# Performance work log

Hardware: AMD Instinct MI355X
Metric: run time of the kernel (lower is better)

Reference implementation:

```python
import jax, jax.numpy as jnp
import numpy as np

BN_EPS = 1e-5

@jax.custom_vjp
def bsign(x):
    # forward: sign(x) (torch semantics: sign(0)=0, matched by jnp.sign)
    return jnp.sign(x)

def _bsign_fwd(x):
    return jnp.sign(x), x

def _bsign_bwd(x, g):
    # straight-through estimator: pass grad where |x| <= 1, zero elsewhere
    return (g * (jnp.abs(x) <= 1.0).astype(g.dtype),)

bsign.defvjp(_bsign_fwd, _bsign_bwd)


def setup_inputs() -> dict:
    key = jax.random.key(0)
    k1, k2 = jax.random.split(key, 2)
    B, IN, OUT = 8192, 2048, 2048
    x = jax.random.normal(k1, (B, IN), dtype=jnp.float32)
    weight = jax.random.normal(k2, (OUT, IN), dtype=jnp.float32) * 0.1
    gamma = jnp.ones((OUT,), dtype=jnp.float32)
    beta = jnp.zeros((OUT,), dtype=jnp.float32)
    return {"x": x, "weight": weight, "gamma": gamma, "beta": beta}


def reference(x, weight, gamma, beta):
    # binarize input and weight to {-1, 0, +1} via sign (STE in bwd)
    xb = bsign(x)            # [B, IN]
    wb = bsign(weight)       # [OUT, IN]
    out = xb @ wb.T          # [B, OUT] full-precision GEMM over +/-1 values
    # BatchNorm1d, training mode: normalize with biased batch statistics
    mean = jnp.mean(out, axis=0)                 # [OUT]
    var = jnp.var(out, axis=0)                   # biased (ddof=0), matches torch BN
    out = (out - mean) * jax.lax.rsqrt(var + BN_EPS) * gamma + beta
    return out
```

## Files before the change

### kernel.cpp

```cpp
#include <hip/hip_runtime.h>
#include <stdint.h>


typedef int int32x4 __attribute__((ext_vector_type(4)));

#define BM 256
#define BN 256
#define BKI 128
#define EPS_BN 1e-5f
#define BAR_STRIDE 32

__device__ __forceinline__ void load16_lds(const void* g, void* l) {
  __builtin_amdgcn_global_load_lds(
      (const __attribute__((address_space(1))) void*)g,
      (__attribute__((address_space(3))) void*)l,
      16, 0, 0);
}

__device__ __forceinline__ char sgn(float v) {
  return v > 0.f ? (char)1 : (v < 0.f ? (char)-1 : (char)0);
}

__global__ void binarize_kernel(const float* __restrict__ x,
                                const float* __restrict__ w,
                                char* __restrict__ Ab, char* __restrict__ Bb,
                                float* __restrict__ stats,
                                int nx4, int ntot4, int n2) {
  int idx = blockIdx.x * blockDim.x + threadIdx.x;
  if (idx < n2) stats[idx] = 0.f;
  if (idx >= ntot4) return;
  const float4* src;
  char* dst;
  int i;
  if (idx < nx4) {
    src = reinterpret_cast<const float4*>(x); dst = Ab; i = idx;
  } else {
    src = reinterpret_cast<const float4*>(w); dst = Bb; i = idx - nx4;
  }
  float4 v = src[i];
  char4 o;
  o.x = sgn(v.x); o.y = sgn(v.y); o.z = sgn(v.z); o.w = sgn(v.w);
  reinterpret_cast<char4*>(dst)[i] = o;
}

__global__ __launch_bounds__(512, 2) void gemm_bn_kernel(
    const char* __restrict__ A,
    const char* __restrict__ Bt,
    float* __restrict__ C,
    float* __restrict__ colSum,
    float* __restrict__ colSq,
    int* __restrict__ barriers,
    const float* __restrict__ gamma,
    const float* __restrict__ beta,
    int M, int N, int K) {
  __shared__ __align__(16) char sA[2][BM * BKI];
  __shared__ __align__(16) char sB[2][BN * BKI];

  const int tid  = threadIdx.x;
  const int wave = tid >> 6;
  const int lane = tid & 63;

  const int nby = M / BM;
  const int panel = blockIdx.x / nby;
  const int rowBlock = (blockIdx.x % nby) * BM;
  const int colBlock = panel * BN;

  const int laneRow = lane >> 3;
  const int cch     = lane & 7;
  const int swz     = ((cch ^ laneRow) & 7) * 16;

  const char* Ag = A  + (size_t)(rowBlock + wave * 32 + laneRow) * K + swz;
  const char* Bg = Bt + (size_t)(colBlock + wave * 32 + laneRow) * K + swz;

  const int f    = lane & 15;
  const int quad = lane >> 4;
  const int f7   = f & 7;
  const int wm = (wave >> 2) * 128;
  const int wn = (wave & 3) * 64;

  int32x4 acc[8][4] = {};

  const int NT = K / BKI;

#pragma unroll
  for (int j = 0; j < 4; ++j) {
    load16_lds(Ag + (size_t)(j * 8) * K, &sA[0][(wave * 32 + j * 8) * BKI]);
    load16_lds(Bg + (size_t)(j * 8) * K, &sB[0][(wave * 32 + j * 8) * BKI]);
  }

  for (int t = 0; t < NT; ++t) {
    const int cur = t & 1;
    const int nxt = cur ^ 1;
    const char* sAc = sA[cur];
    const char* sBc = sB[cur];
    const size_t gkn = (size_t)(t + 1) * BKI;
    const bool pre = (t + 1 < NT);

    __syncthreads();

    int32x4 af[4][2];
#pragma unroll
    for (int q = 0; q < 4; ++q) {
      const int mh = q >> 1, nh = q & 1;
      if (nh == 0) {
#pragma unroll
        for (int mi = 0; mi < 4; ++mi)
#pragma unroll
          for (int s = 0; s < 2; ++s)
            af[mi][s] = *reinterpret_cast<const int32x4*>(
                &sAc[(wm + mh * 64 + mi * 16 + f) * BKI +
                     (((s * 4 + quad) ^ f7) * 16)]);
      }
      int32x4 bf_[2][2];
#pragma unroll
      for (int ni = 0; ni < 2; ++ni)
#pragma unroll
        for (int s = 0; s < 2; ++s)
          bf_[ni][s] = *reinterpret_cast<const int32x4*>(
              &sBc[(wn + nh * 32 + ni * 16 + f) * BKI +
                   (((s * 4 + quad) ^ f7) * 16)]);

      if (pre) {
        if (q < 2) {
#pragma unroll
          for (int j = 0; j < 2; ++j) {
            const int part = q * 2 + j;
            load16_lds(Ag + gkn + (size_t)(part * 8) * K,
                       &sA[nxt][(wave * 32 + part * 8) * BKI]);
          }
        } else {
#pragma unroll
          for (int j = 0; j < 2; ++j) {
            const int part = (q - 2) * 2 + j;
            load16_lds(Bg + gkn + (size_t)(part * 8) * K,
                       &sB[nxt][(wave * 32 + part * 8) * BKI]);
          }
        }
      }

      __builtin_amdgcn_s_barrier();
      __builtin_amdgcn_s_setprio(1);
#pragma unroll
      for (int mi = 0; mi < 4; ++mi)
#pragma unroll
        for (int ni = 0; ni < 2; ++ni)
#pragma unroll
          for (int s = 0; s < 2; ++s)
            acc[mh * 4 + mi][nh * 2 + ni] =
                __builtin_amdgcn_mfma_i32_16x16x64_i8(
                    af[mi][s], bf_[ni][s], acc[mh * 4 + mi][nh * 2 + ni],
                    0, 0, 0);
      __builtin_amdgcn_s_setprio(0);
      __builtin_amdgcn_s_barrier();
    }
  }

#pragma unroll
  for (int in = 0; in < 4; ++in) {
    const int col = colBlock + wn + in * 16 + f;
    float s = 0.f, sq = 0.f;
#pragma unroll
    for (int im = 0; im < 8; ++im)
#pragma unroll
      for (int r = 0; r < 4; ++r) {
        const float fv = (float)acc[im][in][r];
        s += fv;
        sq += fv * fv;
      }
    s  += __shfl_xor(s, 16);  s  += __shfl_xor(s, 32);
    sq += __shfl_xor(sq, 16); sq += __shfl_xor(sq, 32);
    if (quad == 0) {
      atomicAdd(&colSum[col], s);
      atomicAdd(&colSq[col], sq);
    }
  }

  float gmv = 0.f, btv = 0.f;
  if (tid < BN) {
    gmv = gamma[colBlock + tid];
    btv = beta[colBlock + tid];
  }

  __syncthreads();
  if (tid == 0) {
    int* bar = barriers + panel * BAR_STRIDE;
    __hip_atomic_fetch_add(bar, 1, __ATOMIC_RELAXED,
                           __HIP_MEMORY_SCOPE_AGENT);
    while (__hip_atomic_load(bar, __ATOMIC_RELAXED,
                             __HIP_MEMORY_SCOPE_AGENT) < nby) {
      __builtin_amdgcn_s_sleep(8);
    }
    asm volatile("" ::: "memory");
  }
  __syncthreads();

  float2* sSC = reinterpret_cast<float2*>(&sA[0][0]);
  if (tid < BN) {
    const int col = colBlock + tid;
    const float s  = __hip_atomic_load(&colSum[col], __ATOMIC_RELAXED,
                                       __HIP_MEMORY_SCOPE_AGENT);
    const float sq = __hip_atomic_load(&colSq[col], __ATOMIC_RELAXED,
                                       __HIP_MEMORY_SCOPE_AGENT);
    const float invM = 1.0f / (float)M;
    const float mu  = s * invM;
    const float var = sq * invM - mu * mu;
    const float sc  = gmv * rsqrtf(var + EPS_BN);
    const float sh  = btv - mu * sc;
    sSC[tid] = make_float2(sc, sh);
  }
  __syncthreads();

#pragma unroll
  for (int in = 0; in < 4; ++in) {
    const int lc  = wn + in * 16 + f;
    const float2 ss = sSC[lc];
    const int col = colBlock + lc;
#pragma unroll
    for (int im = 0; im < 8; ++im) {
      float* Cp = C + (size_t)(rowBlock + wm + im * 16 + quad * 4) * N + col;
#pragma unroll
      for (int r = 0; r < 4; ++r)
        Cp[(size_t)r * N] = (float)acc[im][in][r] * ss.x + ss.y;
    }
  }
}

extern "C" void kernel_launch(void* const* d_in, const int* in_sizes, int n_in,
                              void* d_out, int out_size, void* d_ws,
                              size_t ws_size, hipStream_t stream) {
  const float* x     = (const float*)d_in[0];
  const float* w     = (const float*)d_in[1];
  const float* gamma = (const float*)d_in[2];
  const float* beta  = (const float*)d_in[3];
  float* C = (float*)d_out;

  const int N = in_sizes[2];
  const int K = in_sizes[1] / N;
  const int M = in_sizes[0] / K;

  char* ws = (char*)d_ws;
  char* Abin = ws;
  char* Bbin = ws + (size_t)M * K;
  float* stats = (float*)(ws + (size_t)M * K + (size_t)N * K);
  float* colSum = stats;
  float* colSq  = stats + N;
  int* barriers = (int*)(stats + 2 * N);

  {
    int nx4 = (M * K) / 4;
    int ntot4 = (M * K + N * K) / 4;
    binarize_kernel<<<(ntot4 + 255) / 256, 256, 0, stream>>>(
        x, w, Abin, Bbin, stats, nx4, ntot4, 2 * N + 16 * BAR_STRIDE);
  }

  {
    const int nTiles = (M / BM) * (N / BN);
    gemm_bn_kernel<<<nTiles, 512, 0, stream>>>(Abin, Bbin, C, colSum, colSq,
                                               barriers, gamma, beta, M, N, K);
  }
}
```

Baseline: 165.1 us.

## Switch int8 GEMM from 16x16x64 to 32x32x32 MFMA tiles

Replaces the 16x16x64 int8 MFMA fragments with 32x32x32 ones. Each wave now computes 4x2 accumulators of 32x32 instead of 8x4 of 16x16. B fragments are loaded once per K tile and A fragments once per 32-row slice, which changes LDS read volume and the fragment register footprint. The BN statistics reduction and the output store indexing are rewritten for the 32x32 accumulator layout. This may cut LDS traffic and instruction count per FLOP, but it changes register pressure and the store access pattern.

```diff
diff --git a/kernel.cpp b/kernel.cpp
--- a/kernel.cpp
+++ b/kernel.cpp
@@ -3,6 +3,7 @@
 
 
 typedef int int32x4 __attribute__((ext_vector_type(4)));
+typedef int int32x16 __attribute__((ext_vector_type(16)));
 
 #define BM 256
 #define BN 256
@@ -72,13 +73,12 @@
   const char* Ag = A  + (size_t)(rowBlock + wave * 32 + laneRow) * K + swz;
   const char* Bg = Bt + (size_t)(colBlock + wave * 32 + laneRow) * K + swz;
 
-  const int f    = lane & 15;
-  const int quad = lane >> 4;
-  const int f7   = f & 7;
+  const int lane31 = lane & 31;
+  const int hi     = lane >> 5;
   const int wm = (wave >> 2) * 128;
   const int wn = (wave & 3) * 64;
 
-  int32x4 acc[8][4] = {};
+  int32x16 acc[4][2] = {};
 
   const int NT = K / BKI;
 
@@ -98,27 +98,28 @@
 
     __syncthreads();
 
-    int32x4 af[4][2];
+    int32x16 bf_[2];
+    int32x4* bfv = reinterpret_cast<int32x4*>(&bf_[0]);
+#pragma unroll
+    for (int ni = 0; ni < 2; ++ni) {
+      const int row = wn + ni * 32 + lane31;
+#pragma unroll
+      for (int ks = 0; ks < 4; ++ks) {
+        const int chunk = ((ks * 2 + hi) ^ (row & 7)) * 16;
+        bfv[ni * 4 + ks] = *reinterpret_cast<const int32x4*>(
+            &sBc[row * BKI + chunk]);
+      }
+    }
+
 #pragma unroll
     for (int q = 0; q < 4; ++q) {
-      const int mh = q >> 1, nh = q & 1;
-      if (nh == 0) {
-#pragma unroll
-        for (int mi = 0; mi < 4; ++mi)
-#pragma unroll
-          for (int s = 0; s < 2; ++s)
-            af[mi][s] = *reinterpret_cast<const int32x4*>(
-                &sAc[(wm + mh * 64 + mi * 16 + f) * BKI +
-                     (((s * 4 + quad) ^ f7) * 16)]);
-      }
-      int32x4 bf_[2][2];
-#pragma unroll
-      for (int ni = 0; ni < 2; ++ni)
-#pragma unroll
-        for (int s = 0; s < 2; ++s)
-          bf_[ni][s] = *reinterpret_cast<const int32x4*>(
-              &sBc[(wn + nh * 32 + ni * 16 + f) * BKI +
-                   (((s * 4 + quad) ^ f7) * 16)]);
+      int32x4 af[4];
+      const int arow = wm + q * 32 + lane31;
+#pragma unroll
+      for (int ks = 0; ks < 4; ++ks) {
+        const int chunk = ((ks * 2 + hi) ^ (arow & 7)) * 16;
+        af[ks] = *reinterpret_cast<const int32x4*>(&sAc[arow * BKI + chunk]);
+      }
 
       if (pre) {
         if (q < 2) {
@@ -141,35 +142,31 @@
       __builtin_amdgcn_s_barrier();
       __builtin_amdgcn_s_setprio(1);
 #pragma unroll
-      for (int mi = 0; mi < 4; ++mi)
+      for (int ks = 0; ks < 4; ++ks)
 #pragma unroll
         for (int ni = 0; ni < 2; ++ni)
-#pragma unroll
-          for (int s = 0; s < 2; ++s)
-            acc[mh * 4 + mi][nh * 2 + ni] =
-                __builtin_amdgcn_mfma_i32_16x16x64_i8(
-                    af[mi][s], bf_[ni][s], acc[mh * 4 + mi][nh * 2 + ni],
-                    0, 0, 0);
+          acc[q][ni] = __builtin_amdgcn_mfma_i32_32x32x32_i8(
+              af[ks], bfv[ni * 4 + ks], acc[q][ni], 0, 0, 0);
       __builtin_amdgcn_s_setprio(0);
       __builtin_amdgcn_s_barrier();
     }
   }
 
 #pragma unroll
-  for (int in = 0; in < 4; ++in) {
-    const int col = colBlock + wn + in * 16 + f;
+  for (int ni = 0; ni < 2; ++ni) {
+    const int col = colBlock + wn + ni * 32 + lane31;
     float s = 0.f, sq = 0.f;
 #pragma unroll
-    for (int im = 0; im < 8; ++im)
-#pragma unroll
-      for (int r = 0; r < 4; ++r) {
-        const float fv = (float)acc[im][in][r];
+    for (int mi = 0; mi < 4; ++mi)
+#pragma unroll
+      for (int r = 0; r < 16; ++r) {
+        const float fv = (float)acc[mi][ni][r];
         s += fv;
         sq += fv * fv;
       }
-    s  += __shfl_xor(s, 16);  s  += __shfl_xor(s, 32);
-    sq += __shfl_xor(sq, 16); sq += __shfl_xor(sq, 32);
-    if (quad == 0) {
+    s  += __shfl_xor(s, 32);
+    sq += __shfl_xor(sq, 32);
+    if (hi == 0) {
       atomicAdd(&colSum[col], s);
       atomicAdd(&colSq[col], sq);
     }
@@ -211,16 +208,18 @@
   __syncthreads();
 
 #pragma unroll
-  for (int in = 0; in < 4; ++in) {
-    const int lc  = wn + in * 16 + f;
+  for (int ni = 0; ni < 2; ++ni) {
+    const int lc  = wn + ni * 32 + lane31;
     const float2 ss = sSC[lc];
     const int col = colBlock + lc;
 #pragma unroll
-    for (int im = 0; im < 8; ++im) {
-      float* Cp = C + (size_t)(rowBlock + wm + im * 16 + quad * 4) * N + col;
-#pragma unroll
-      for (int r = 0; r < 4; ++r)
-        Cp[(size_t)r * N] = (float)acc[im][in][r] * ss.x + ss.y;
+    for (int mi = 0; mi < 4; ++mi) {
+#pragma unroll
+      for (int r = 0; r < 16; ++r) {
+        const int row = rowBlock + wm + mi * 32 + (r & 3) + 8 * (r >> 2) +
+                        4 * hi;
+        C[(size_t)row * N + col] = (float)acc[mi][ni][r] * ss.x + ss.y;
+      }
     }
   }
 }
```

Result: no change. 164.9 us (-0.1%).
